# Kernel optimization log

Hardware: AMD Instinct MI355X
Metric: run time of the kernel (lower is better)

The kernel has to match this reference:

```python
import jax, jax.numpy as jnp
import numpy as np

HID = 8
EMB = 32


def setup_inputs() -> dict:
    V = 32000
    S, B = 128, 32
    key = jax.random.key(0)
    ks = jax.random.split(key, 13)
    u = lambda k, shape, s: jax.random.uniform(k, shape, jnp.float32, -1.0 / np.sqrt(s), 1.0 / np.sqrt(s))
    return {
        "input_batch": jax.random.randint(ks[0], (S, B), 0, V, dtype=jnp.int64),
        "lookup": u(ks[1], (V, EMB), EMB),
        "weight_xf": u(ks[2], (EMB, HID), HID),
        "weight_hf": u(ks[3], (HID, HID), HID),
        "weight_xb": u(ks[4], (EMB, HID), HID),
        "weight_hb": u(ks[5], (HID, HID), HID),
        "weight_o": u(ks[6], (2 * HID, V), V),
        "Hf": u(ks[7], (HID,), HID),
        "Hb": u(ks[8], (HID,), HID),
        "bias_x": u(ks[9], (HID,), HID),
        "bias_hf": u(ks[10], (HID,), HID),
        "bias_hb": u(ks[11], (HID,), HID),
        "bias_o": u(ks[12], (V,), V),
    }


def reference(input_batch, lookup, weight_xf, weight_hf, weight_xb, weight_hb,
              weight_o, Hf, Hb, bias_x, bias_hf, bias_hb, bias_o):
    S, B = input_batch.shape
    X = lookup[input_batch]  # [S, B, EMB]

    # Forward Elman scan. Hf_table[i] = hidden BEFORE consuming x[i] (shifted).
    h0f = jnp.broadcast_to(Hf, (B, HID))

    def fstep(h, x):
        h2 = jnp.tanh(x @ weight_xf + bias_x + h @ weight_hf + bias_hf)
        return h2, h2

    _, hf = jax.lax.scan(fstep, h0f, X)
    Hf_table = jnp.concatenate([h0f[None], hf[:-1]], axis=0)  # [S, B, HID]

    # Backward Elman scan (reverse). hb[i] = hidden after consuming x[i..S-1];
    # original uses hidden after x[i+1..S-1] at position i (init at i=S-1).
    h0b = jnp.broadcast_to(Hb, (B, HID))

    def bstep(h, x):
        h2 = jnp.tanh(x @ weight_xb + bias_x + h @ weight_hb + bias_hb)
        return h2, h2

    _, hb = jax.lax.scan(bstep, h0b, X, reverse=True)
    Hb_table = jnp.concatenate([hb[1:], h0b[None]], axis=0)  # [S, B, HID]

    H = jnp.concatenate([Hf_table, Hb_table], axis=-1)  # [S, B, 2*HID]
    logits = H @ weight_o + bias_o  # [S, B, V]
    return jax.nn.log_softmax(logits, axis=-1)
```

## Files before the change

kernel.cpp:

```cpp
#include <hip/hip_runtime.h>
#include <hip/hip_bf16.h>

#define S_LEN 128
#define B_SZ  32
#define VOCAB 32000
#define EMB   32
#define HID   8
#define NROWS 4096

typedef float v2f __attribute__((ext_vector_type(2)));
typedef float v4f __attribute__((ext_vector_type(4)));

#if defined(__has_builtin) && __has_builtin(__builtin_elementwise_fma)
__device__ __forceinline__ v2f fma2(v2f a, v2f b, v2f c) {
    return __builtin_elementwise_fma(a, b, c);
}
#else
__device__ __forceinline__ v2f fma2(v2f a, v2f b, v2f c) {
    v2f r; r.x = fmaf(a.x, b.x, c.x); r.y = fmaf(a.y, b.y, c.y); return r;
}
#endif

__global__ __launch_bounds__(256) void prep_kernel(
        const int* __restrict__ idx,
        const float* __restrict__ lookup,
        const float* __restrict__ wxf,
        const float* __restrict__ wxb,
        const float* __restrict__ bias_x,
        const float* __restrict__ bias_hf,
        const float* __restrict__ bias_hb,
        float* __restrict__ xpF, float* __restrict__ xpB,
        const float* __restrict__ wo, float* __restrict__ wo_p) {
    int blk = blockIdx.x;
    if (blk < 16) {
        int tok = blk * 256 + threadIdx.x;
        int e = idx[tok];
        const float* xr = lookup + (size_t)e * EMB;
        float x[EMB];
        #pragma unroll
        for (int i = 0; i < EMB; ++i) x[i] = xr[i];
        #pragma unroll
        for (int j = 0; j < HID; ++j) {
            float bx = bias_x[j];
            float fa = bx + bias_hf[j];
            float fb = bx + bias_hb[j];
            #pragma unroll
            for (int e2 = 0; e2 < EMB; ++e2) {
                float xv = x[e2];
                fa += xv * wxf[e2 * HID + j];
                fb += xv * wxb[e2 * HID + j];
            }
            xpF[(size_t)tok * HID + j] = fa;
            xpB[(size_t)tok * HID + j] = fb;
        }
    } else {
        int v2 = (blk - 16) * 256 + threadIdx.x;
        if (v2 >= VOCAB / 2) return;
        float2 buf[16];
        #pragma unroll
        for (int k = 0; k < 16; ++k)
            buf[k] = *reinterpret_cast<const float2*>(wo + (size_t)k * VOCAB + 2 * v2);
        float4* dst = reinterpret_cast<float4*>(wo_p + (size_t)v2 * 32);
        #pragma unroll
        for (int q = 0; q < 8; ++q)
            dst[q] = make_float4(buf[2 * q].x, buf[2 * q].y,
                                 buf[2 * q + 1].x, buf[2 * q + 1].y);
    }
}

__global__ __launch_bounds__(64) void scan_kernel(
        const float* __restrict__ xpF,
        const float* __restrict__ xpB,
        const float* __restrict__ whf,
        const float* __restrict__ whb,
        const float* __restrict__ Hf0,
        const float* __restrict__ Hb0,
        float* __restrict__ Hws) {
    int gtid = blockIdx.x * 64 + threadIdx.x;
    int j   = gtid & 7;
    int b   = (gtid >> 3) & 31;
    int dir = gtid >> 8;

    const float* wh = dir ? whb : whf;
    float w[HID];
    #pragma unroll
    for (int k = 0; k < HID; ++k) w[k] = wh[k * HID + j];

    const float* xp = dir ? xpB : xpF;
    float h = dir ? Hb0[j] : Hf0[j];

    int s0 = dir ? (S_LEN - 1) : 0;
    float xv = xp[(size_t)(s0 * B_SZ + b) * HID + j];

    for (int step = 0; step < S_LEN; ++step) {
        int s = dir ? (S_LEN - 1 - step) : step;
        int r = s * B_SZ + b;
        float xv_next = 0.0f;
        if (step + 1 < S_LEN) {
            int sn = dir ? (S_LEN - 2 - step) : (step + 1);
            xv_next = xp[(size_t)(sn * B_SZ + b) * HID + j];
        }
        Hws[(size_t)r * 16 + dir * HID + j] = h;
        float acc = xv;
        #pragma unroll
        for (int k = 0; k < HID; ++k)
            acc += __shfl(h, k, 8) * w[k];
        float ex = __expf(2.0f * acc);
        h = 1.0f - 2.0f * __builtin_amdgcn_rcpf(ex + 1.0f);
        xv = xv_next;
    }
}

#define VCH_A 256
#define NCH_A (VOCAB / VCH_A)
__global__ __launch_bounds__(256) void passA_kernel(
        const float* __restrict__ Hws,
        const float* __restrict__ wo_p,
        const float* __restrict__ bias_o,
        float* __restrict__ Zpart) {
    int ra = blockIdx.y * 256 + threadIdx.x;
    int rb = ra + (NROWS / 2);
    int p0 = blockIdx.x * (VCH_A / 2);

    float ha[16], hb[16];
    const float4* ha4 = reinterpret_cast<const float4*>(Hws + (size_t)ra * 16);
    const float4* hb4 = reinterpret_cast<const float4*>(Hws + (size_t)rb * 16);
    #pragma unroll
    for (int q = 0; q < 4; ++q) {
        float4 fa = ha4[q];
        float4 fb = hb4[q];
        ha[4 * q + 0] = fa.x; ha[4 * q + 1] = fa.y;
        ha[4 * q + 2] = fa.z; ha[4 * q + 3] = fa.w;
        hb[4 * q + 0] = fb.x; hb[4 * q + 1] = fb.y;
        hb[4 * q + 2] = fb.z; hb[4 * q + 3] = fb.w;
    }

    float za = 0.0f, zb = 0.0f;
    #pragma unroll 2
    for (int p = 0; p < VCH_A / 2; ++p) {
        const v2f* wp = reinterpret_cast<const v2f*>(wo_p + (size_t)(p0 + p) * 32);
        float2 bb = *reinterpret_cast<const float2*>(bias_o + (size_t)(p0 + p) * 2);
        v2f acca; acca.x = bb.x; acca.y = bb.y;
        v2f accb = acca;
        #pragma unroll
        for (int k = 0; k < 16; ++k) {
            v2f w = wp[k];
            v2f hka; hka.x = ha[k]; hka.y = ha[k];
            v2f hkb; hkb.x = hb[k]; hkb.y = hb[k];
            acca = fma2(hka, w, acca);
            accb = fma2(hkb, w, accb);
        }
        za += __expf(acca.x) + __expf(acca.y);
        zb += __expf(accb.x) + __expf(accb.y);
    }
    Zpart[(size_t)blockIdx.x * NROWS + ra] = za;
    Zpart[(size_t)blockIdx.x * NROWS + rb] = zb;
}

__global__ __launch_bounds__(256) void logz_kernel(
        const float* __restrict__ Zpart, float* __restrict__ logZ) {
    int r = blockIdx.x * blockDim.x + threadIdx.x;
    if (r >= NROWS) return;
    float s = 0.0f;
    for (int i = 0; i < NCH_A; ++i) s += Zpart[(size_t)i * NROWS + r];
    logZ[r] = logf(s);
}

#define MT_B 128
__global__ __launch_bounds__(256) void passB_kernel(
        const float* __restrict__ Hws,
        const float* __restrict__ wo,
        const float* __restrict__ bias_o,
        const float* __restrict__ logZ,
        float* __restrict__ out) {
    __shared__ __attribute__((aligned(16))) float hsh[MT_B * 16];
    __shared__ float lz_sh[MT_B];
    int t = threadIdx.x;
    int r0 = blockIdx.y * MT_B;

    {
        const float4* src = reinterpret_cast<const float4*>(Hws + (size_t)r0 * 16);
        float4* dst = reinterpret_cast<float4*>(hsh);
        dst[t]       = src[t];
        dst[t + 256] = src[t + 256];
        if (t < MT_B) lz_sh[t] = logZ[r0 + t];
    }
    __syncthreads();

    int v = (blockIdx.x * 256 + t) * 4;
    if (v < VOCAB) {
        v2f w01[16], w23[16];
        #pragma unroll
        for (int k = 0; k < 16; ++k) {
            float4 w4 = *reinterpret_cast<const float4*>(wo + (size_t)k * VOCAB + v);
            w01[k].x = w4.x; w01[k].y = w4.y;
            w23[k].x = w4.z; w23[k].y = w4.w;
        }
        float4 bv = *reinterpret_cast<const float4*>(bias_o + v);
        v2f b01; b01.x = bv.x; b01.y = bv.y;
        v2f b23; b23.x = bv.z; b23.y = bv.w;

        #pragma unroll 2
        for (int rr = 0; rr < MT_B; ++rr) {
            const float* hr = hsh + rr * 16;
            v2f t01 = b01, t23 = b23;
            #pragma unroll
            for (int k = 0; k < 16; ++k) {
                float hk = hr[k];
                v2f hk2; hk2.x = hk; hk2.y = hk;
                t01 = fma2(hk2, w01[k], t01);
                t23 = fma2(hk2, w23[k], t23);
            }
            float lz = lz_sh[rr];
            v4f o;
            o.x = t01.x - lz; o.y = t01.y - lz;
            o.z = t23.x - lz; o.w = t23.y - lz;
            __builtin_nontemporal_store(
                o, reinterpret_cast<v4f*>(out + (size_t)(r0 + rr) * VOCAB + v));
        }
    }
}

extern "C" void kernel_launch(void* const* d_in, const int* in_sizes, int n_in,
                              void* d_out, int out_size, void* d_ws, size_t ws_size,
                              hipStream_t stream) {
    const int*   idx     = (const int*)d_in[0];
    const float* lookup  = (const float*)d_in[1];
    const float* wxf     = (const float*)d_in[2];
    const float* whf     = (const float*)d_in[3];
    const float* wxb     = (const float*)d_in[4];
    const float* whb     = (const float*)d_in[5];
    const float* wo      = (const float*)d_in[6];
    const float* Hf0     = (const float*)d_in[7];
    const float* Hb0     = (const float*)d_in[8];
    const float* bias_x  = (const float*)d_in[9];
    const float* bias_hf = (const float*)d_in[10];
    const float* bias_hb = (const float*)d_in[11];
    const float* bias_o  = (const float*)d_in[12];
    float* out = (float*)d_out;

    float* ws    = (float*)d_ws;
    float* xpF   = ws;
    float* xpB   = ws + 32768;
    float* Hws   = ws + 65536;
    float* wo_p  = ws + 131072;
    float* Zpart = ws + 643072;
    float* logZ  = ws + 1155072;

    prep_kernel<<<79, 256, 0, stream>>>(idx, lookup, wxf, wxb,
                                        bias_x, bias_hf, bias_hb,
                                        xpF, xpB, wo, wo_p);
    scan_kernel<<<8, 64, 0, stream>>>(xpF, xpB, whf, whb, Hf0, Hb0, Hws);
    passA_kernel<<<dim3(NCH_A, 8), 256, 0, stream>>>(Hws, wo_p, bias_o, Zpart);
    logz_kernel<<<16, 256, 0, stream>>>(Zpart, logZ);
    passB_kernel<<<dim3(32, NROWS / MT_B), 256, 0, stream>>>(Hws, wo, bias_o, logZ, out);
}
```

Baseline: 659.3 us.

## Fuse prep and scan kernels, fold logZ into passB, 4 rows per passA thread

```diff
diff --git a/kernel.cpp b/kernel.cpp
--- a/kernel.cpp
+++ b/kernel.cpp
@@ -21,94 +21,97 @@
 }
 #endif
 
-__global__ __launch_bounds__(256) void prep_kernel(
+#define XP_STRIDE 65
+__global__ __launch_bounds__(256) void fused_pre_kernel(
         const int* __restrict__ idx,
         const float* __restrict__ lookup,
         const float* __restrict__ wxf,
         const float* __restrict__ wxb,
-        const float* __restrict__ bias_x,
-        const float* __restrict__ bias_hf,
-        const float* __restrict__ bias_hb,
-        float* __restrict__ xpF, float* __restrict__ xpB,
-        const float* __restrict__ wo, float* __restrict__ wo_p) {
-    int blk = blockIdx.x;
-    if (blk < 16) {
-        int tok = blk * 256 + threadIdx.x;
-        int e = idx[tok];
-        const float* xr = lookup + (size_t)e * EMB;
-        float x[EMB];
-        #pragma unroll
-        for (int i = 0; i < EMB; ++i) x[i] = xr[i];
-        #pragma unroll
-        for (int j = 0; j < HID; ++j) {
-            float bx = bias_x[j];
-            float fa = bx + bias_hf[j];
-            float fb = bx + bias_hb[j];
-            #pragma unroll
-            for (int e2 = 0; e2 < EMB; ++e2) {
-                float xv = x[e2];
-                fa += xv * wxf[e2 * HID + j];
-                fb += xv * wxb[e2 * HID + j];
-            }
-            xpF[(size_t)tok * HID + j] = fa;
-            xpB[(size_t)tok * HID + j] = fb;
-        }
-    } else {
-        int v2 = (blk - 16) * 256 + threadIdx.x;
-        if (v2 >= VOCAB / 2) return;
-        float2 buf[16];
-        #pragma unroll
-        for (int k = 0; k < 16; ++k)
-            buf[k] = *reinterpret_cast<const float2*>(wo + (size_t)k * VOCAB + 2 * v2);
-        float4* dst = reinterpret_cast<float4*>(wo_p + (size_t)v2 * 32);
-        #pragma unroll
-        for (int q = 0; q < 8; ++q)
-            dst[q] = make_float4(buf[2 * q].x, buf[2 * q].y,
-                                 buf[2 * q + 1].x, buf[2 * q + 1].y);
-    }
-}
-
-__global__ __launch_bounds__(64) void scan_kernel(
-        const float* __restrict__ xpF,
-        const float* __restrict__ xpB,
         const float* __restrict__ whf,
         const float* __restrict__ whb,
         const float* __restrict__ Hf0,
         const float* __restrict__ Hb0,
+        const float* __restrict__ bias_x,
+        const float* __restrict__ bias_hf,
+        const float* __restrict__ bias_hb,
+        const float* __restrict__ wo,
+        float* __restrict__ wo_p,
         float* __restrict__ Hws) {
-    int gtid = blockIdx.x * 64 + threadIdx.x;
-    int j   = gtid & 7;
-    int b   = (gtid >> 3) & 31;
-    int dir = gtid >> 8;
-
-    const float* wh = dir ? whb : whf;
-    float w[HID];
-    #pragma unroll
-    for (int k = 0; k < HID; ++k) w[k] = wh[k * HID + j];
-
-    const float* xp = dir ? xpB : xpF;
-    float h = dir ? Hb0[j] : Hf0[j];
-
-    int s0 = dir ? (S_LEN - 1) : 0;
-    float xv = xp[(size_t)(s0 * B_SZ + b) * HID + j];
-
-    for (int step = 0; step < S_LEN; ++step) {
-        int s = dir ? (S_LEN - 1 - step) : step;
-        int r = s * B_SZ + b;
-        float xv_next = 0.0f;
-        if (step + 1 < S_LEN) {
-            int sn = dir ? (S_LEN - 2 - step) : (step + 1);
-            xv_next = xp[(size_t)(sn * B_SZ + b) * HID + j];
-        }
-        Hws[(size_t)r * 16 + dir * HID + j] = h;
-        float acc = xv;
-        #pragma unroll
-        for (int k = 0; k < HID; ++k)
-            acc += __shfl(h, k, 8) * w[k];
-        float ex = __expf(2.0f * acc);
-        h = 1.0f - 2.0f * __builtin_amdgcn_rcpf(ex + 1.0f);
-        xv = xv_next;
-    }
+    __shared__ float xp[S_LEN * XP_STRIDE];
+    int t = threadIdx.x;
+
+    if (blockIdx.x < 8) {
+        int blk   = blockIdx.x;
+        int dir   = blk >> 2;
+        int bbase = (blk & 3) * 8;
+        const float* wx = dir ? wxb : wxf;
+        const float* bh = dir ? bias_hb : bias_hf;
+
+        {
+            int s   = t >> 1;
+            int bh4 = (t & 1) * 4;
+            #pragma unroll
+            for (int bb = 0; bb < 4; ++bb) {
+                int bl = bh4 + bb;
+                int e = idx[s * B_SZ + bbase + bl];
+                const float4* xr4 =
+                    reinterpret_cast<const float4*>(lookup + (size_t)e * EMB);
+                float x[EMB];
+                #pragma unroll
+                for (int q = 0; q < 8; ++q) {
+                    float4 f = xr4[q];
+                    x[4 * q + 0] = f.x; x[4 * q + 1] = f.y;
+                    x[4 * q + 2] = f.z; x[4 * q + 3] = f.w;
+                }
+                #pragma unroll
+                for (int j = 0; j < HID; ++j) {
+                    float fa = bias_x[j] + bh[j];
+                    #pragma unroll
+                    for (int e2 = 0; e2 < EMB; ++e2)
+                        fa += x[e2] * wx[e2 * HID + j];
+                    xp[s * XP_STRIDE + bl * HID + j] = fa;
+                }
+            }
+        }
+        __syncthreads();
+
+        if (t < 64) {
+            int j  = t & 7;
+            int bl = t >> 3;
+            int b  = bbase + bl;
+            const float* wh = dir ? whb : whf;
+            float w[HID];
+            #pragma unroll
+            for (int k = 0; k < HID; ++k) w[k] = wh[k * HID + j];
+            float h = dir ? Hb0[j] : Hf0[j];
+
+            for (int step = 0; step < S_LEN; ++step) {
+                int s = dir ? (S_LEN - 1 - step) : step;
+                float xv = xp[s * XP_STRIDE + bl * HID + j];
+                int r = s * B_SZ + b;
+                Hws[(size_t)r * 16 + dir * HID + j] = h;
+                float acc = xv;
+                #pragma unroll
+                for (int k = 0; k < HID; ++k)
+                    acc += __shfl(h, k, 8) * w[k];
+                float ex = __expf(2.0f * acc);
+                h = 1.0f - 2.0f * __builtin_amdgcn_rcpf(ex + 1.0f);
+            }
+        }
+        return;
+    }
+
+    int v2 = (blockIdx.x - 8) * 256 + t;
+    if (v2 >= VOCAB / 2) return;
+    float2 buf[16];
+    #pragma unroll
+    for (int k = 0; k < 16; ++k)
+        buf[k] = *reinterpret_cast<const float2*>(wo + (size_t)k * VOCAB + 2 * v2);
+    float4* dst = reinterpret_cast<float4*>(wo_p + (size_t)v2 * 32);
+    #pragma unroll
+    for (int q = 0; q < 8; ++q)
+        dst[q] = make_float4(buf[2 * q].x, buf[2 * q].y,
+                             buf[2 * q + 1].x, buf[2 * q + 1].y);
 }
 
 #define VCH_A 256
@@ -118,52 +121,46 @@
         const float* __restrict__ wo_p,
         const float* __restrict__ bias_o,
         float* __restrict__ Zpart) {
-    int ra = blockIdx.y * 256 + threadIdx.x;
-    int rb = ra + (NROWS / 2);
+    int r0 = blockIdx.y * 256 + threadIdx.x;
     int p0 = blockIdx.x * (VCH_A / 2);
 
-    float ha[16], hb[16];
-    const float4* ha4 = reinterpret_cast<const float4*>(Hws + (size_t)ra * 16);
-    const float4* hb4 = reinterpret_cast<const float4*>(Hws + (size_t)rb * 16);
-    #pragma unroll
-    for (int q = 0; q < 4; ++q) {
-        float4 fa = ha4[q];
-        float4 fb = hb4[q];
-        ha[4 * q + 0] = fa.x; ha[4 * q + 1] = fa.y;
-        ha[4 * q + 2] = fa.z; ha[4 * q + 3] = fa.w;
-        hb[4 * q + 0] = fb.x; hb[4 * q + 1] = fb.y;
-        hb[4 * q + 2] = fb.z; hb[4 * q + 3] = fb.w;
-    }
-
-    float za = 0.0f, zb = 0.0f;
+    float h[4][16];
+    #pragma unroll
+    for (int rr = 0; rr < 4; ++rr) {
+        const float4* h4 =
+            reinterpret_cast<const float4*>(Hws + (size_t)(r0 + 1024 * rr) * 16);
+        #pragma unroll
+        for (int q = 0; q < 4; ++q) {
+            float4 f = h4[q];
+            h[rr][4 * q + 0] = f.x; h[rr][4 * q + 1] = f.y;
+            h[rr][4 * q + 2] = f.z; h[rr][4 * q + 3] = f.w;
+        }
+    }
+
+    float z[4] = {0.0f, 0.0f, 0.0f, 0.0f};
     #pragma unroll 2
     for (int p = 0; p < VCH_A / 2; ++p) {
         const v2f* wp = reinterpret_cast<const v2f*>(wo_p + (size_t)(p0 + p) * 32);
         float2 bb = *reinterpret_cast<const float2*>(bias_o + (size_t)(p0 + p) * 2);
-        v2f acca; acca.x = bb.x; acca.y = bb.y;
-        v2f accb = acca;
+        v2f acc[4];
+        #pragma unroll
+        for (int rr = 0; rr < 4; ++rr) { acc[rr].x = bb.x; acc[rr].y = bb.y; }
         #pragma unroll
         for (int k = 0; k < 16; ++k) {
             v2f w = wp[k];
-            v2f hka; hka.x = ha[k]; hka.y = ha[k];
-            v2f hkb; hkb.x = hb[k]; hkb.y = hb[k];
-            acca = fma2(hka, w, acca);
-            accb = fma2(hkb, w, accb);
-        }
-        za += __expf(acca.x) + __expf(acca.y);
-        zb += __expf(accb.x) + __expf(accb.y);
-    }
-    Zpart[(size_t)blockIdx.x * NROWS + ra] = za;
-    Zpart[(size_t)blockIdx.x * NROWS + rb] = zb;
-}
-
-__global__ __launch_bounds__(256) void logz_kernel(
-        const float* __restrict__ Zpart, float* __restrict__ logZ) {
-    int r = blockIdx.x * blockDim.x + threadIdx.x;
-    if (r >= NROWS) return;
-    float s = 0.0f;
-    for (int i = 0; i < NCH_A; ++i) s += Zpart[(size_t)i * NROWS + r];
-    logZ[r] = logf(s);
+            #pragma unroll
+            for (int rr = 0; rr < 4; ++rr) {
+                v2f hk; hk.x = h[rr][k]; hk.y = h[rr][k];
+                acc[rr] = fma2(hk, w, acc[rr]);
+            }
+        }
+        #pragma unroll
+        for (int rr = 0; rr < 4; ++rr)
+            z[rr] += __expf(acc[rr].x) + __expf(acc[rr].y);
+    }
+    #pragma unroll
+    for (int rr = 0; rr < 4; ++rr)
+        Zpart[(size_t)blockIdx.x * NROWS + r0 + 1024 * rr] = z[rr];
 }
 
 #define MT_B 128
@@ -171,7 +168,7 @@
         const float* __restrict__ Hws,
         const float* __restrict__ wo,
         const float* __restrict__ bias_o,
-        const float* __restrict__ logZ,
+        const float* __restrict__ Zpart,
         float* __restrict__ out) {
     __shared__ __attribute__((aligned(16))) float hsh[MT_B * 16];
     __shared__ float lz_sh[MT_B];
@@ -183,7 +180,12 @@
         float4* dst = reinterpret_cast<float4*>(hsh);
         dst[t]       = src[t];
         dst[t + 256] = src[t + 256];
-        if (t < MT_B) lz_sh[t] = logZ[r0 + t];
+        if (t < MT_B) {
+            float s = 0.0f;
+            for (int i = 0; i < NCH_A; ++i)
+                s += Zpart[(size_t)i * NROWS + r0 + t];
+            lz_sh[t] = logf(s);
+        }
     }
     __syncthreads();
 
@@ -240,18 +242,14 @@
     float* out = (float*)d_out;
 
     float* ws    = (float*)d_ws;
-    float* xpF   = ws;
-    float* xpB   = ws + 32768;
-    float* Hws   = ws + 65536;
-    float* wo_p  = ws + 131072;
-    float* Zpart = ws + 643072;
-    float* logZ  = ws + 1155072;
-
-    prep_kernel<<<79, 256, 0, stream>>>(idx, lookup, wxf, wxb,
-                                        bias_x, bias_hf, bias_hb,
-                                        xpF, xpB, wo, wo_p);
-    scan_kernel<<<8, 64, 0, stream>>>(xpF, xpB, whf, whb, Hf0, Hb0, Hws);
-    passA_kernel<<<dim3(NCH_A, 8), 256, 0, stream>>>(Hws, wo_p, bias_o, Zpart);
-    logz_kernel<<<16, 256, 0, stream>>>(Zpart, logZ);
-    passB_kernel<<<dim3(32, NROWS / MT_B), 256, 0, stream>>>(Hws, wo, bias_o, logZ, out);
-}
+    float* Hws   = ws;
+    float* wo_p  = ws + 65536;
+    float* Zpart = ws + 577536;
+
+    fused_pre_kernel<<<71, 256, 0, stream>>>(idx, lookup, wxf, wxb, whf, whb,
+                                             Hf0, Hb0, bias_x, bias_hf, bias_hb,
+                                             wo, wo_p, Hws);
+    passA_kernel<<<dim3(NCH_A, 4), 256, 0, stream>>>(Hws, wo_p, bias_o, Zpart);
+    passB_kernel<<<dim3(32, NROWS / MT_B), 256, 0, stream>>>(Hws, wo, bias_o,
+                                                             Zpart, out);
+}
```

Result: no change. 661.0 us (+0.3%).
